# Optimization experiments

Hardware: AMD Instinct MI355X
Metric: run time of the kernel (lower is better)

Reference implementation:

```python
import jax, jax.numpy as jnp
import numpy as np

RADIUS = 6
KERNEL = 2 * RADIUS + 1  # 13
TEMPERATURE = 0.07
EPS = 1e-12  # F.normalize eps


def setup_inputs() -> dict:
    key = jax.random.key(0)
    k1, k2 = jax.random.split(key)
    B, C, H, W = 4, 256, 128, 128
    f_a = jax.random.normal(k1, (B, C, H, W), dtype=jnp.float32)
    f_b = jax.random.normal(k2, (B, C, H, W), dtype=jnp.float32)
    return {"f_a": f_a, "f_b": f_b}


def _l2_normalize(x):
    # matches F.normalize(x, dim=1): x / max(||x||_2, eps)
    n = jnp.sqrt(jnp.sum(x * x, axis=1, keepdims=True))
    return x / jnp.maximum(n, EPS)


def reference(f_a, f_b):
    a = _l2_normalize(f_a)
    b = _l2_normalize(f_b)
    b_pad = jnp.pad(b, ((0, 0), (0, 0), (RADIUS, RADIUS), (RADIUS, RADIUS)))

    # offsets in the same (row-major ky, kx) order as F.unfold
    ky, kx = jnp.meshgrid(jnp.arange(KERNEL), jnp.arange(KERNEL), indexing="ij")
    offsets = jnp.stack([ky.ravel(), kx.ravel()], axis=-1)  # [K^2, 2]

    shape = f_a.shape  # (B, C, H, W)

    def step(carry, off):
        shifted = jax.lax.dynamic_slice(b_pad, (0, 0, off[0], off[1]), shape)
        c = jnp.einsum("bchw,bchw->bhw", a, shifted)
        return carry, c

    _, corr = jax.lax.scan(step, None, offsets)  # [K^2, B, H, W]
    corr = jnp.transpose(corr, (1, 0, 2, 3)) / TEMPERATURE  # [B, K^2, H, W]
    return corr
```

## Files before the change

### kernel.cpp

```cpp
#include <hip/hip_runtime.h>
#include <stdint.h>


typedef _Float16 half8 __attribute__((ext_vector_type(8)));
typedef float floatx4 __attribute__((ext_vector_type(4)));

#define B_ 4
#define C_ 256
#define H_ 128
#define W_ 128
#define K2_ 169
#define INV_T 14.285714285714286f
#define HW_ (H_ * W_)

union SmemU { _Float16 stage[2][16384]; float ostage[K2_ * 2 * 17]; };

__global__ __launch_bounds__(512, 4) void corr_fused(const float* __restrict__ fa,
                                                     const float* __restrict__ fb,
                                                     float* __restrict__ out) {
  __shared__ SmemU u;
  __shared__ float inv_b[448];
  __shared__ float inv_a[64];
  const int bid = blockIdx.x;
  const int xcd = bid & 7, l = bid >> 3;
  const int bb = l >> 5, hseg = (l >> 3) & 3, wt = l & 7;
  const int hg = xcd * 4 + hseg;
  const int h0 = hg * 4, w0 = wt * 16;
  const int t = threadIdx.x;
  const int lane = t & 63, wv = t >> 6;
  const int ml = lane & 15, q = lane >> 4;
  const int ntile = wv & 1, jjg = wv >> 1;

  bool ok;
  const float* gp;
  int pxo;
  if (t < 448) {
    const int row = t / 28, col = t - row * 28;
    const int rim = h0 - 6 + row, cim = w0 - 6 + col;
    ok = ((unsigned)rim < (unsigned)H_) && ((unsigned)cim < (unsigned)W_);
    gp = fb + (size_t)bb * C_ * HW_ + (ok ? (rim * W_ + cim) : 0);
    pxo = t * 32;
  } else {
    const int px = t - 448;
    const int r = px >> 4, m = px & 15;
    ok = true;
    gp = fa + (size_t)bb * C_ * HW_ + (h0 + r) * W_ + (w0 + m);
    pxo = 14336 + px * 32;
  }

  float ss = 0.f;
  float v[32];

  #pragma unroll
  for (int cc = 0; cc < 32; ++cc) v[cc] = ok ? gp[(size_t)cc * HW_] : 0.f;
  gp += (size_t)32 * HW_;
  {
    _Float16* wb = u.stage[0] + pxo;
    #pragma unroll
    for (int qq = 0; qq < 4; ++qq) {
      half8 hh;
      #pragma unroll
      for (int j = 0; j < 8; ++j) { const float x = v[qq * 8 + j]; ss += x * x; hh[j] = (_Float16)x; }
      *(half8*)(wb + qq * 8) = hh;
    }
  }

  floatx4 acc[4][4] = {};

  for (int kg = 0; kg < 8; ++kg) {
    if (kg < 7) {
      #pragma unroll
      for (int cc = 0; cc < 32; ++cc) v[cc] = ok ? gp[(size_t)cc * HW_] : 0.f;
      gp += (size_t)32 * HW_;
    }
    __syncthreads();
    const _Float16* sb = u.stage[kg & 1];

    half8 A[4];
    #pragma unroll
    for (int r = 0; r < 4; ++r)
      A[r] = *(const half8*)(sb + 14336 + (r * 16 + ml) * 32 + q * 8);

    #pragma unroll
    for (int uu = 0; uu < 4; ++uu) {
      const int jj = jjg + 4 * uu;
      const half8 Bf = *(const half8*)(sb + jj * 896 + (ntile * 16 + ml) * 32 + q * 8);
      #pragma unroll
      for (int r = 0; r < 4; ++r) {
        if ((uu == 0 && r > jjg) || (uu == 3 && r < jjg)) continue;
        acc[uu][r] = __builtin_amdgcn_mfma_f32_16x16x32_f16(A[r], Bf, acc[uu][r], 0, 0, 0);
      }
    }

    if (kg < 7) {
      _Float16* wb = u.stage[(kg + 1) & 1] + pxo;
      #pragma unroll
      for (int qq = 0; qq < 4; ++qq) {
        half8 hh;
        #pragma unroll
        for (int j = 0; j < 8; ++j) { const float x = v[qq * 8 + j]; ss += x * x; hh[j] = (_Float16)x; }
        *(half8*)(wb + qq * 8) = hh;
      }
    }
  }

  if (t < 448) inv_b[t] = 1.0f / fmaxf(sqrtf(ss), 1e-12f);
  else         inv_a[t - 448] = INV_T / fmaxf(sqrtf(ss), 1e-12f);
  __syncthreads();

  #pragma unroll
  for (int r2 = 0; r2 < 2; ++r2) {
    if (r2) __syncthreads();
    #pragma unroll
    for (int uu = 0; uu < 4; ++uu) {
      const int jj = jjg + 4 * uu;
      const int col = ntile * 16 + ml;
      const float sbv = (col < 28) ? inv_b[jj * 28 + col] : 0.f;
      #pragma unroll
      for (int rr = 2 * r2; rr < 2 * r2 + 2; ++rr) {
        if ((uu == 0 && rr > jjg) || (uu == 3 && rr < jjg)) continue;
        const int dy6 = jj - rr;
        #pragma unroll
        for (int p = 0; p < 4; ++p) {
          const int ip = q * 4 + p;
          const int dx6 = col - ip;
          if (dx6 >= 0 && dx6 <= 12)
            u.ostage[((dy6 * 13 + dx6) * 2 + (rr & 1)) * 17 + ip] =
                acc[uu][rr][p] * sbv * inv_a[rr * 16 + ip];
        }
      }
    }
    __syncthreads();
    for (int s = t; s < K2_ * 32; s += 512) {
      const int k = s >> 5, r1 = (s >> 4) & 1, ip = s & 15;
      out[(((size_t)bb * K2_ + k) * H_ + h0 + 2 * r2 + r1) * W_ + w0 + ip] =
          u.ostage[(k * 2 + r1) * 17 + ip];
    }
  }
}

extern "C" void kernel_launch(void* const* d_in, const int* in_sizes, int n_in,
                              void* d_out, int out_size, void* d_ws, size_t ws_size,
                              hipStream_t stream) {
  const float* fa = (const float*)d_in[0];
  const float* fb = (const float*)d_in[1];
  float* out = (float*)d_out;
  (void)d_ws; (void)ws_size;
  corr_fused<<<1024, 512, 0, stream>>>(fa, fb, out);
}
```

Baseline: 210.9 us.

## Hand-schedule global loads with inline asm and partial vmcnt waits

Replaces the compiler-generated prefetch loads with inline-asm global_load_dword and packs each 8-channel chunk after a partial s_waitcnt vmcnt, so conversion and LDS stores start before all 32 loads land. The per-iteration __syncthreads is replaced by an explicit lgkmcnt wait plus s_barrier after the LDS writes, the k-group loop is fully unrolled, and launch bounds drop from 4 to 2 waves per SIMD to allow more registers. Out-of-bounds pixels now load from a clamped address and are zeroed at pack time. The risks are lower occupancy and losing the compiler's ability to reorder around the asm and sched barriers.

```diff
diff --git a/kernel.cpp b/kernel.cpp
--- a/kernel.cpp
+++ b/kernel.cpp
@@ -15,7 +15,20 @@
 
 union SmemU { _Float16 stage[2][16384]; float ostage[K2_ * 2 * 17]; };
 
-__global__ __launch_bounds__(512, 4) void corr_fused(const float* __restrict__ fa,
+#define PACK_CHUNK(WB, QQ, NW)                                                  \
+  do {                                                                          \
+    asm volatile("s_waitcnt vmcnt(" #NW ")" ::: "memory");                      \
+    __builtin_amdgcn_sched_barrier(0);                                          \
+    half8 hh;                                                                   \
+    _Pragma("unroll") for (int j = 0; j < 8; ++j) {                             \
+      const float x = ok ? vv[(QQ) * 8 + j] : 0.f;                              \
+      ss += x * x;                                                              \
+      hh[j] = (_Float16)x;                                                      \
+    }                                                                           \
+    *(half8*)((WB) + (QQ) * 8) = hh;                                            \
+  } while (0)
+
+__global__ __launch_bounds__(512, 2) void corr_fused(const float* __restrict__ fa,
                                                      const float* __restrict__ fb,
                                                      float* __restrict__ out) {
   __shared__ SmemU u;
@@ -49,33 +62,36 @@
   }
 
   float ss = 0.f;
-  float v[32];
+  float vv[32];
 
   #pragma unroll
-  for (int cc = 0; cc < 32; ++cc) v[cc] = ok ? gp[(size_t)cc * HW_] : 0.f;
+  for (int cc = 0; cc < 32; ++cc)
+    asm volatile("global_load_dword %0, %1, off" : "=v"(vv[cc]) : "v"(gp + (size_t)cc * HW_));
   gp += (size_t)32 * HW_;
   {
     _Float16* wb = u.stage[0] + pxo;
-    #pragma unroll
-    for (int qq = 0; qq < 4; ++qq) {
-      half8 hh;
-      #pragma unroll
-      for (int j = 0; j < 8; ++j) { const float x = v[qq * 8 + j]; ss += x * x; hh[j] = (_Float16)x; }
-      *(half8*)(wb + qq * 8) = hh;
-    }
+    PACK_CHUNK(wb, 0, 24);
+    PACK_CHUNK(wb, 1, 16);
+    PACK_CHUNK(wb, 2, 8);
+    PACK_CHUNK(wb, 3, 0);
   }
+  asm volatile("s_waitcnt lgkmcnt(0)" ::: "memory");
+  __builtin_amdgcn_sched_barrier(0);
+  __builtin_amdgcn_s_barrier();
+  __builtin_amdgcn_sched_barrier(0);
 
   floatx4 acc[4][4] = {};
 
+  #pragma unroll
   for (int kg = 0; kg < 8; ++kg) {
     if (kg < 7) {
       #pragma unroll
-      for (int cc = 0; cc < 32; ++cc) v[cc] = ok ? gp[(size_t)cc * HW_] : 0.f;
+      for (int cc = 0; cc < 32; ++cc)
+        asm volatile("global_load_dword %0, %1, off" : "=v"(vv[cc]) : "v"(gp + (size_t)cc * HW_));
       gp += (size_t)32 * HW_;
     }
-    __syncthreads();
+
     const _Float16* sb = u.stage[kg & 1];
-
     half8 A[4];
     #pragma unroll
     for (int r = 0; r < 4; ++r)
@@ -94,13 +110,14 @@
 
     if (kg < 7) {
       _Float16* wb = u.stage[(kg + 1) & 1] + pxo;
-      #pragma unroll
-      for (int qq = 0; qq < 4; ++qq) {
-        half8 hh;
-        #pragma unroll
-        for (int j = 0; j < 8; ++j) { const float x = v[qq * 8 + j]; ss += x * x; hh[j] = (_Float16)x; }
-        *(half8*)(wb + qq * 8) = hh;
-      }
+      PACK_CHUNK(wb, 0, 24);
+      PACK_CHUNK(wb, 1, 16);
+      PACK_CHUNK(wb, 2, 8);
+      PACK_CHUNK(wb, 3, 0);
+      asm volatile("s_waitcnt lgkmcnt(0)" ::: "memory");
+      __builtin_amdgcn_sched_barrier(0);
+      __builtin_amdgcn_s_barrier();
+      __builtin_amdgcn_sched_barrier(0);
     }
   }
 
```

Measured after the change: 365.0 us. +73.1%, slower.

## Split channel loads across four threads per pixel and interleave with MFMAs

Applied to the files above, without the earlier changes.

Each thread now loads 8 channels for four pixels (strided by 128) instead of 32 channels for one pixel. The prefetch of the next channel chunk is split into two halves that are interleaved between MFMA groups, which halves the per-thread register buffer and lets the global loads overlap the matrix work. The per-pixel sum of squares is reduced across the four sub-lanes with shuffles before the norms are computed. Each thread now carries more address and predicate state, and the new access pattern may coalesce less well.

```diff
diff --git a/kernel.cpp b/kernel.cpp
--- a/kernel.cpp
+++ b/kernel.cpp
@@ -15,6 +15,40 @@
 
 union SmemU { _Float16 stage[2][16384]; float ostage[K2_ * 2 * 17]; };
 
+#define LOAD_HALF(HH)                                                          \
+  do {                                                                         \
+    _Pragma("unroll") for (int g_ = 2 * (HH); g_ < 2 * (HH) + 2; ++g_) {       \
+      _Pragma("unroll") for (int j_ = 0; j_ < 8; ++j_)                         \
+        vv[(g_ & 1) * 8 + j_] = okg[g_] ? gp[g_][(size_t)j_ * HW_] : 0.f;      \
+      gp[g_] += (size_t)32 * HW_;                                              \
+    }                                                                          \
+  } while (0)
+
+#define PACK_HALF(WB, HH)                                                      \
+  do {                                                                         \
+    _Pragma("unroll") for (int g_ = 2 * (HH); g_ < 2 * (HH) + 2; ++g_) {       \
+      half8 hh_;                                                               \
+      _Pragma("unroll") for (int j_ = 0; j_ < 8; ++j_) {                       \
+        const float x_ = vv[(g_ & 1) * 8 + j_];                                \
+        ssg[g_] += x_ * x_;                                                    \
+        hh_[j_] = (_Float16)x_;                                                \
+      }                                                                        \
+      *(half8*)((WB) + pxo[g_]) = hh_;                                         \
+    }                                                                          \
+  } while (0)
+
+#define MFMA_UU(UU)                                                            \
+  do {                                                                         \
+    const int jj_ = jjg + 4 * (UU);                                            \
+    const half8 Bf_ =                                                          \
+        *(const half8*)(sb + jj_ * 896 + (ntile * 16 + ml) * 32 + q * 8);      \
+    _Pragma("unroll") for (int r = 0; r < 4; ++r) {                            \
+      if (((UU) == 0 && r > jjg) || ((UU) == 3 && r < jjg)) continue;          \
+      acc[(UU)][r] =                                                           \
+          __builtin_amdgcn_mfma_f32_16x16x32_f16(A[r], Bf_, acc[(UU)][r], 0, 0, 0); \
+    }                                                                          \
+  } while (0)
+
 __global__ __launch_bounds__(512, 4) void corr_fused(const float* __restrict__ fa,
                                                      const float* __restrict__ fb,
                                                      float* __restrict__ out) {
@@ -31,81 +65,74 @@
   const int ml = lane & 15, q = lane >> 4;
   const int ntile = wv & 1, jjg = wv >> 1;
 
-  bool ok;
-  const float* gp;
-  int pxo;
-  if (t < 448) {
-    const int row = t / 28, col = t - row * 28;
-    const int rim = h0 - 6 + row, cim = w0 - 6 + col;
-    ok = ((unsigned)rim < (unsigned)H_) && ((unsigned)cim < (unsigned)W_);
-    gp = fb + (size_t)bb * C_ * HW_ + (ok ? (rim * W_ + cim) : 0);
-    pxo = t * 32;
-  } else {
-    const int px = t - 448;
-    const int r = px >> 4, m = px & 15;
-    ok = true;
-    gp = fa + (size_t)bb * C_ * HW_ + (h0 + r) * W_ + (w0 + m);
-    pxo = 14336 + px * 32;
+  const int p0 = t >> 2, sub = t & 3;
+  const float* gp[4];
+  bool okg[4];
+  int pxo[4];
+  #pragma unroll
+  for (int g = 0; g < 4; ++g) {
+    const int px = p0 + 128 * g;
+    pxo[g] = px * 32 + sub * 8;
+    if (px < 448) {
+      const int row = px / 28, col = px - row * 28;
+      const int rim = h0 - 6 + row, cim = w0 - 6 + col;
+      okg[g] = ((unsigned)rim < (unsigned)H_) && ((unsigned)cim < (unsigned)W_);
+      gp[g] = fb + (size_t)bb * C_ * HW_ + (size_t)(sub * 8) * HW_ +
+              (okg[g] ? (rim * W_ + cim) : 0);
+    } else {
+      const int ap = px - 448;
+      const int r = ap >> 4, m = ap & 15;
+      okg[g] = true;
+      gp[g] = fa + (size_t)bb * C_ * HW_ + (size_t)(sub * 8) * HW_ +
+              (h0 + r) * W_ + (w0 + m);
+    }
   }
 
-  float ss = 0.f;
-  float v[32];
+  float ssg[4] = {0.f, 0.f, 0.f, 0.f};
+  float vv[16];
 
-  #pragma unroll
-  for (int cc = 0; cc < 32; ++cc) v[cc] = ok ? gp[(size_t)cc * HW_] : 0.f;
-  gp += (size_t)32 * HW_;
-  {
-    _Float16* wb = u.stage[0] + pxo;
-    #pragma unroll
-    for (int qq = 0; qq < 4; ++qq) {
-      half8 hh;
-      #pragma unroll
-      for (int j = 0; j < 8; ++j) { const float x = v[qq * 8 + j]; ss += x * x; hh[j] = (_Float16)x; }
-      *(half8*)(wb + qq * 8) = hh;
-    }
-  }
+  LOAD_HALF(0);
+  PACK_HALF(u.stage[0], 0);
+  LOAD_HALF(1);
+  PACK_HALF(u.stage[0], 1);
 
   floatx4 acc[4][4] = {};
 
   for (int kg = 0; kg < 8; ++kg) {
-    if (kg < 7) {
-      #pragma unroll
-      for (int cc = 0; cc < 32; ++cc) v[cc] = ok ? gp[(size_t)cc * HW_] : 0.f;
-      gp += (size_t)32 * HW_;
-    }
     __syncthreads();
     const _Float16* sb = u.stage[kg & 1];
+    _Float16* wb = u.stage[(kg + 1) & 1];
+    const bool pf = (kg < 7);
+
+    if (pf) LOAD_HALF(0);
 
     half8 A[4];
     #pragma unroll
     for (int r = 0; r < 4; ++r)
       A[r] = *(const half8*)(sb + 14336 + (r * 16 + ml) * 32 + q * 8);
 
+    MFMA_UU(0);
+    if (pf) { PACK_HALF(wb, 0); LOAD_HALF(1); }
+    MFMA_UU(1);
+    MFMA_UU(2);
+    if (pf) PACK_HALF(wb, 1);
+    MFMA_UU(3);
+  }
+
+  #pragma unroll
+  for (int g = 0; g < 4; ++g) {
+    ssg[g] += __shfl_xor(ssg[g], 1, 64);
+    ssg[g] += __shfl_xor(ssg[g], 2, 64);
+  }
+  if (sub == 0) {
     #pragma unroll
-    for (int uu = 0; uu < 4; ++uu) {
-      const int jj = jjg + 4 * uu;
-      const half8 Bf = *(const half8*)(sb + jj * 896 + (ntile * 16 + ml) * 32 + q * 8);
-      #pragma unroll
-      for (int r = 0; r < 4; ++r) {
-        if ((uu == 0 && r > jjg) || (uu == 3 && r < jjg)) continue;
-        acc[uu][r] = __builtin_amdgcn_mfma_f32_16x16x32_f16(A[r], Bf, acc[uu][r], 0, 0, 0);
-      }
-    }
-
-    if (kg < 7) {
-      _Float16* wb = u.stage[(kg + 1) & 1] + pxo;
-      #pragma unroll
-      for (int qq = 0; qq < 4; ++qq) {
-        half8 hh;
-        #pragma unroll
-        for (int j = 0; j < 8; ++j) { const float x = v[qq * 8 + j]; ss += x * x; hh[j] = (_Float16)x; }
-        *(half8*)(wb + qq * 8) = hh;
-      }
+    for (int g = 0; g < 4; ++g) {
+      const int px = p0 + 128 * g;
+      const float inv = 1.0f / fmaxf(sqrtf(ssg[g]), 1e-12f);
+      if (px < 448) inv_b[px] = inv;
+      else          inv_a[px - 448] = INV_T * inv;
     }
   }
-
-  if (t < 448) inv_b[t] = 1.0f / fmaxf(sqrtf(ss), 1e-12f);
-  else         inv_a[t - 448] = INV_T / fmaxf(sqrtf(ss), 1e-12f);
   __syncthreads();
 
   #pragma unroll
```

New measurement: 256.2 us. 1.21x slower.

## Stage fp32 tiles into LDS with direct global-to-LDS DMA and swizzled layout

Applied to the files above, without the earlier changes.

Replaces the register-staged load, convert-to-fp16 and LDS write with global_load_lds DMA that copies fp32 channel slices straight into a double-buffered, XOR-swizzled LDS tile, 16 channels per phase. Operands are converted to fp16 at fragment-read time and fed to the 16x16x16 MFMA instead of 16x16x32. The squared-norm accumulation is now read from LDS. The aim is to cut VGPR pressure and register round-trips and to overlap loads with compute. In exchange it doubles the number of phases and barriers, uses fp32 LDS traffic and 4-byte DMA granularity, and zeroes out-of-bounds inv_b instead of the loaded values.

```diff
diff --git a/kernel.cpp b/kernel.cpp
--- a/kernel.cpp
+++ b/kernel.cpp
@@ -2,7 +2,7 @@
 #include <stdint.h>
 
 
-typedef _Float16 half8 __attribute__((ext_vector_type(8)));
+typedef _Float16 half4v __attribute__((ext_vector_type(4)));
 typedef float floatx4 __attribute__((ext_vector_type(4)));
 
 #define B_ 4
@@ -12,8 +12,31 @@
 #define K2_ 169
 #define INV_T 14.285714285714286f
 #define HW_ (H_ * W_)
+#define CPP 16
+#define NPH 16
 
-union SmemU { _Float16 stage[2][16384]; float ostage[K2_ * 2 * 17]; };
+union SmemU { float stage[2][512 * CPP]; float ostage[K2_ * 2 * 17]; };
+
+static __device__ __forceinline__ void dma4(const float* g, float* l) {
+  __builtin_amdgcn_global_load_lds((const __attribute__((address_space(1))) void*)g,
+                                   (__attribute__((address_space(3))) void*)l, 4, 0, 0);
+}
+
+#define ISSUE_DMA(PH, NB)                                                      \
+  do {                                                                         \
+    float* db_ = u.stage[NB] + wv * 64 * CPP;      \
+    const float* pb_ = base + (size_t)(PH) * CPP * HW_;                        \
+    _Pragma("unroll") for (int i_ = 0; i_ < 16; ++i_)                          \
+      dma4(pb_ + off[i_], db_ + i_ * 64);                                      \
+  } while (0)
+
+#define PHASE_BARRIER()                                                        \
+  do {                                                                         \
+    asm volatile("s_waitcnt vmcnt(0)" ::: "memory");                           \
+    __builtin_amdgcn_sched_barrier(0);                                         \
+    __builtin_amdgcn_s_barrier();                                              \
+    __builtin_amdgcn_sched_barrier(0);                                         \
+  } while (0)
 
 __global__ __launch_bounds__(512, 4) void corr_fused(const float* __restrict__ fa,
                                                      const float* __restrict__ fb,
@@ -31,80 +54,76 @@
   const int ml = lane & 15, q = lane >> 4;
   const int ntile = wv & 1, jjg = wv >> 1;
 
-  bool ok;
-  const float* gp;
-  int pxo;
+  const int csl = ((((lane & 15) >> 2) ^ (lane >> 4)) << 2) + (lane & 3);
+  const float* srcw = (wv == 7) ? fa : fb;
+  const float* base = srcw + (size_t)bb * C_ * HW_ + (size_t)csl * HW_;
+  int off[16];
+  #pragma unroll
+  for (int i = 0; i < 16; ++i) {
+    const int px = wv * 64 + i * 4 + (lane >> 4);
+    int io;
+    if (px < 448) {
+      const int row = px / 28, col = px - row * 28;
+      const int rim = h0 - 6 + row, cim = w0 - 6 + col;
+      const bool okp = ((unsigned)rim < (unsigned)H_) && ((unsigned)cim < (unsigned)W_);
+      io = okp ? (rim * W_ + cim) : 0;
+    } else {
+      const int ap = px - 448;
+      io = (h0 + (ap >> 4)) * W_ + (w0 + (ap & 15));
+    }
+    off[i] = io;
+  }
+
+  bool own_ok = true;
   if (t < 448) {
     const int row = t / 28, col = t - row * 28;
     const int rim = h0 - 6 + row, cim = w0 - 6 + col;
-    ok = ((unsigned)rim < (unsigned)H_) && ((unsigned)cim < (unsigned)W_);
-    gp = fb + (size_t)bb * C_ * HW_ + (ok ? (rim * W_ + cim) : 0);
-    pxo = t * 32;
-  } else {
-    const int px = t - 448;
-    const int r = px >> 4, m = px & 15;
-    ok = true;
-    gp = fa + (size_t)bb * C_ * HW_ + (h0 + r) * W_ + (w0 + m);
-    pxo = 14336 + px * 32;
+    own_ok = ((unsigned)rim < (unsigned)H_) && ((unsigned)cim < (unsigned)W_);
   }
 
-  float ss = 0.f;
-  float v[32];
-
-  #pragma unroll
-  for (int cc = 0; cc < 32; ++cc) v[cc] = ok ? gp[(size_t)cc * HW_] : 0.f;
-  gp += (size_t)32 * HW_;
-  {
-    _Float16* wb = u.stage[0] + pxo;
-    #pragma unroll
-    for (int qq = 0; qq < 4; ++qq) {
-      half8 hh;
-      #pragma unroll
-      for (int j = 0; j < 8; ++j) { const float x = v[qq * 8 + j]; ss += x * x; hh[j] = (_Float16)x; }
-      *(half8*)(wb + qq * 8) = hh;
-    }
-  }
+  ISSUE_DMA(0, 0);
+  PHASE_BARRIER();
 
   floatx4 acc[4][4] = {};
+  float ss = 0.f;
 
-  for (int kg = 0; kg < 8; ++kg) {
-    if (kg < 7) {
-      #pragma unroll
-      for (int cc = 0; cc < 32; ++cc) v[cc] = ok ? gp[(size_t)cc * HW_] : 0.f;
-      gp += (size_t)32 * HW_;
+  for (int ph = 0; ph < NPH; ++ph) {
+    if (ph < NPH - 1) ISSUE_DMA(ph + 1, (ph + 1) & 1);
+
+    const float* sb = u.stage[ph & 1];
+
+    half4v A[4];
+    #pragma unroll
+    for (int r = 0; r < 4; ++r) {
+      const floatx4 f =
+          *(const floatx4*)(sb + (448 + r * 16 + ml) * CPP + ((q ^ (ml & 3)) << 2));
+      A[r] = half4v{(_Float16)f.x, (_Float16)f.y, (_Float16)f.z, (_Float16)f.w};
     }
-    __syncthreads();
-    const _Float16* sb = u.stage[kg & 1];
-
-    half8 A[4];
-    #pragma unroll
-    for (int r = 0; r < 4; ++r)
-      A[r] = *(const half8*)(sb + 14336 + (r * 16 + ml) * 32 + q * 8);
 
     #pragma unroll
     for (int uu = 0; uu < 4; ++uu) {
       const int jj = jjg + 4 * uu;
-      const half8 Bf = *(const half8*)(sb + jj * 896 + (ntile * 16 + ml) * 32 + q * 8);
+      const int brow = jj * 28 + ntile * 16 + ml;
+      const floatx4 f =
+          *(const floatx4*)(sb + brow * CPP + ((q ^ (ml & 3)) << 2));
+      const half4v Bf = half4v{(_Float16)f.x, (_Float16)f.y, (_Float16)f.z, (_Float16)f.w};
       #pragma unroll
       for (int r = 0; r < 4; ++r) {
         if ((uu == 0 && r > jjg) || (uu == 3 && r < jjg)) continue;
-        acc[uu][r] = __builtin_amdgcn_mfma_f32_16x16x32_f16(A[r], Bf, acc[uu][r], 0, 0, 0);
+        acc[uu][r] = __builtin_amdgcn_mfma_f32_16x16x16f16(A[r], Bf, acc[uu][r], 0, 0, 0);
       }
     }
 
-    if (kg < 7) {
-      _Float16* wb = u.stage[(kg + 1) & 1] + pxo;
-      #pragma unroll
-      for (int qq = 0; qq < 4; ++qq) {
-        half8 hh;
-        #pragma unroll
-        for (int j = 0; j < 8; ++j) { const float x = v[qq * 8 + j]; ss += x * x; hh[j] = (_Float16)x; }
-        *(half8*)(wb + qq * 8) = hh;
-      }
+    #pragma unroll
+    for (int k = 0; k < 4; ++k) {
+      const floatx4 f = *(const floatx4*)(sb + t * CPP + (((k + t) & 3) << 2));
+      ss += f.x * f.x + f.y * f.y + f.z * f.z + f.w * f.w;
     }
+
+    if (ph < NPH - 1) PHASE_BARRIER();
   }
 
-  if (t < 448) inv_b[t] = 1.0f / fmaxf(sqrtf(ss), 1e-12f);
+  if (t < 448) inv_b[t] = own_ok ? (1.0f / fmaxf(sqrtf(ss), 1e-12f)) : 0.f;
   else         inv_a[t - 448] = INV_T / fmaxf(sqrtf(ss), 1e-12f);
   __syncthreads();
 
```

New measurement: 379.0 us. 79.7% more time.
